# Kernel tuning notes

Measured on AMD Instinct MI355X. Metric: run time of the kernel, lower is better.

## Reference

```python
import jax, jax.numpy as jnp
import numpy as np

B, S, T, E = 16, 512, 128, 256
VIN, VOUT, ENC, DEC = 32000, 32000, 32, 128


def pos_encoding(length, depth):
    # standard sinusoidal positional encoding (TF tutorial / AddPositionalEmbedding)
    half = depth // 2
    pos = jnp.arange(length, dtype=jnp.float32)[:, None]          # (L,1)
    rates = (1.0 / (10000.0 ** (jnp.arange(half, dtype=jnp.float32) / half)))[None, :]
    ang = pos * rates                                             # (L, depth/2)
    return jnp.concatenate([jnp.sin(ang), jnp.cos(ang)], axis=-1)  # (L, depth)


def lstm_scan(x, W, U, b, reverse=False):
    # Keras LSTM, gate order i,f,g,o; zero initial state. x: (B,S,E) -> (B,S,H), h_final
    Bn, H = x.shape[0], U.shape[0]
    def step(carry, xt):
        h, c = carry
        z = xt @ W + h @ U + b
        i, f, g, o = jnp.split(z, 4, axis=-1)
        c = jax.nn.sigmoid(f) * c + jax.nn.sigmoid(i) * jnp.tanh(g)
        h = jax.nn.sigmoid(o) * jnp.tanh(c)
        return (h, c), h
    h0 = jnp.zeros((Bn, H), x.dtype)
    (h, _), hs = jax.lax.scan(step, (h0, h0), jnp.swapaxes(x, 0, 1), reverse=reverse)
    return jnp.swapaxes(hs, 0, 1), h


def setup_inputs() -> dict:
    key = jax.random.key(0)
    ks = jax.random.split(key, 20)
    s = 0.05
    return {
        'source': jax.random.randint(ks[0], (B, S), 0, VIN, dtype=jnp.int32),
        'target': jax.random.randint(ks[1], (B, T), 0, VOUT, dtype=jnp.int32),
        'src_emb': jax.random.normal(ks[2], (VIN, E), jnp.float32) * s,
        'tgt_emb': jax.random.normal(ks[3], (VOUT, E), jnp.float32) * s,
        'Wf': jax.random.normal(ks[4], (E, 4 * ENC), jnp.float32) * s,
        'Uf': jax.random.normal(ks[5], (ENC, 4 * ENC), jnp.float32) * s,
        'bf': jnp.zeros((4 * ENC,), jnp.float32),
        'Wb': jax.random.normal(ks[6], (E, 4 * ENC), jnp.float32) * s,
        'Ub': jax.random.normal(ks[7], (ENC, 4 * ENC), jnp.float32) * s,
        'bb': jnp.zeros((4 * ENC,), jnp.float32),
        'W1': jax.random.normal(ks[8], (2 * ENC, DEC), jnp.float32) * s,
        'b1': jnp.zeros((DEC,), jnp.float32),
        'W2': jax.random.normal(ks[9], (2 * ENC, DEC), jnp.float32) * s,
        'b2': jnp.zeros((DEC,), jnp.float32),
        'Vw': jax.random.normal(ks[10], (DEC, 1), jnp.float32) * s,
        'Vb': jnp.zeros((1,), jnp.float32),
        'Wd': jax.random.normal(ks[11], (2 * ENC + E, 4 * DEC), jnp.float32) * s,
        'bd': jnp.zeros((4 * DEC,), jnp.float32),
        'Wfc': jax.random.normal(ks[12], (DEC, VOUT), jnp.float32) * s,
        'bfc': jnp.zeros((VOUT,), jnp.float32),
    }


def reference(source, target, src_emb, tgt_emb, Wf, Uf, bf, Wb, Ub, bb,
              W1, b1, W2, b2, Vw, Vb, Wd, bd, Wfc, bfc):
    # source embedding + positional encoding
    src = src_emb[source] * jnp.sqrt(jnp.float32(E)) + pos_encoding(S, E)  # (B,S,E)
    # bidirectional encoder (enc_units=32 each direction)
    out_f, hf = lstm_scan(src, Wf, Uf, bf)
    out_b, hb = lstm_scan(src, Wb, Ub, bb, reverse=True)
    enc = jnp.concatenate([out_f, out_b], axis=-1)        # (B,S,64)
    hidden = jnp.concatenate([hf, hb], axis=-1)           # (B,64) — constant query
    # Bahdanau attention with constant query -> constant context vector
    score = jnp.tanh(hidden[:, None, :] @ W1 + b1 + enc @ W2 + b2) @ Vw + Vb  # (B,S,1)
    attw = jax.nn.softmax(score, axis=1)
    ctx = jnp.sum(attw * enc, axis=1)                     # (B,64)
    # per-timestep decoder: LSTM restarts from zero state each step, so all
    # T steps are independent -> vectorize single LSTM step over T
    temb = tgt_emb[target]                                # (B,T,E)
    x = jnp.concatenate(
        [jnp.broadcast_to(ctx[:, None, :], (B, T, 2 * ENC)), temb], axis=-1)  # (B,T,320)
    z = x @ Wd + bd
    i, f, g, o = jnp.split(z, 4, axis=-1)
    c = jax.nn.sigmoid(i) * jnp.tanh(g)                   # c_prev = 0 => forget gate inert
    h = jax.nn.sigmoid(o) * jnp.tanh(c)                   # (B,T,128)
    return h @ Wfc + bfc                                  # (B,T,VOUT)
```

## Files before the change

### kernel.cpp

```cpp
#include <hip/hip_runtime.h>
#include <hip/hip_bf16.h>
#include <math.h>

#define BB 16
#define SS 512
#define TT 128
#define EE 256
#define ENC 32
#define DEC 128
#define VOUT 32000

typedef _Float16 half8 __attribute__((ext_vector_type(8)));
typedef float floatx4 __attribute__((ext_vector_type(4)));

__device__ __forceinline__ float sigmoidf_(float x) { return 1.0f / (1.0f + expf(-x)); }

__global__ __launch_bounds__(256) void k_embed_gemm(
    const int* __restrict__ source, const float* __restrict__ src_emb,
    const float* __restrict__ Wf, const float* __restrict__ bf,
    const float* __restrict__ Wb, const float* __restrict__ bb,
    float* __restrict__ Zf, float* __restrict__ Zb)
{
    __shared__ __align__(16) float sSrc[8][EE];
    const int r0 = blockIdx.x * 8;
    const int tid = threadIdx.x;

    for (int idx = tid; idx < 8 * EE; idx += 256) {
        const int r = idx >> 8, e = idx & 255;
        const int row = r0 + r;
        const int s = row & (SS - 1);
        const int tok = source[row];
        float v = src_emb[(size_t)tok * EE + e] * 16.0f;
        const int jh = (e < 128) ? e : (e - 128);
        const float rate = expf(-0.07195578415f * (float)jh);
        const float ang = (float)s * rate;
        v += (e < 128) ? sinf(ang) : cosf(ang);
        sSrc[r][e] = v;
    }
    __syncthreads();

    const int j = tid & 127;
    const float* W = (tid < 128) ? Wf : Wb;
    const float* bv = (tid < 128) ? bf : bb;
    float* Zo = (tid < 128) ? Zf : Zb;

    float acc[8];
    const float bias = bv[j];
#pragma unroll
    for (int r = 0; r < 8; ++r) acc[r] = bias;

    for (int e = 0; e < EE; e += 4) {
        const float w0 = W[(e + 0) * 128 + j];
        const float w1 = W[(e + 1) * 128 + j];
        const float w2 = W[(e + 2) * 128 + j];
        const float w3 = W[(e + 3) * 128 + j];
#pragma unroll
        for (int r = 0; r < 8; ++r) {
            const float4 x = *(const float4*)&sSrc[r][e];
            acc[r] = fmaf(x.x, w0, acc[r]);
            acc[r] = fmaf(x.y, w1, acc[r]);
            acc[r] = fmaf(x.z, w2, acc[r]);
            acc[r] = fmaf(x.w, w3, acc[r]);
        }
    }
#pragma unroll
    for (int r = 0; r < 8; ++r) Zo[(size_t)(r0 + r) * 128 + j] = acc[r];
}

__global__ __launch_bounds__(128) void k_scan(
    const float* __restrict__ Zf, const float* __restrict__ Zb,
    const float* __restrict__ Uf, const float* __restrict__ Ub,
    float* __restrict__ enc, float* __restrict__ hidden)
{
    const int blk = blockIdx.x;
    const int batch = blk >> 1;
    const int dir = blk & 1;
    const float* Z = dir ? Zb : Zf;
    const float* U = dir ? Ub : Uf;
    const int j = threadIdx.x;

    float u[ENC];
#pragma unroll
    for (int k = 0; k < ENC; ++k) u[k] = U[k * 128 + j];

    __shared__ __align__(16) float sh[ENC];
    __shared__ float sc_[ENC];
    __shared__ float sz[128];
    if (j < ENC) { sh[j] = 0.0f; sc_[j] = 0.0f; }
    __syncthreads();

    const float* Zp = Z + (size_t)batch * (SS * 128) + j;
    float zin = Zp[(dir ? (SS - 1) : 0) * 128];

    for (int step = 0; step < SS; ++step) {
        const int t = dir ? (SS - 1 - step) : step;
        float acc0 = zin;
        if (step < SS - 1) {
            const int tn = dir ? (SS - 2 - step) : (step + 1);
            zin = Zp[tn * 128];
        }
        float acc1 = 0.f, acc2 = 0.f, acc3 = 0.f;
        {
            const float4 h0 = *(const float4*)&sh[0];
            const float4 h1 = *(const float4*)&sh[4];
            const float4 h2 = *(const float4*)&sh[8];
            const float4 h3 = *(const float4*)&sh[12];
            const float4 h4 = *(const float4*)&sh[16];
            const float4 h5 = *(const float4*)&sh[20];
            const float4 h6 = *(const float4*)&sh[24];
            const float4 h7 = *(const float4*)&sh[28];
            acc0 = fmaf(h0.x, u[0], acc0);  acc0 = fmaf(h0.y, u[1], acc0);
            acc0 = fmaf(h0.z, u[2], acc0);  acc0 = fmaf(h0.w, u[3], acc0);
            acc1 = fmaf(h1.x, u[4], acc1);  acc1 = fmaf(h1.y, u[5], acc1);
            acc1 = fmaf(h1.z, u[6], acc1);  acc1 = fmaf(h1.w, u[7], acc1);
            acc2 = fmaf(h2.x, u[8], acc2);  acc2 = fmaf(h2.y, u[9], acc2);
            acc2 = fmaf(h2.z, u[10], acc2); acc2 = fmaf(h2.w, u[11], acc2);
            acc3 = fmaf(h3.x, u[12], acc3); acc3 = fmaf(h3.y, u[13], acc3);
            acc3 = fmaf(h3.z, u[14], acc3); acc3 = fmaf(h3.w, u[15], acc3);
            acc0 = fmaf(h4.x, u[16], acc0); acc0 = fmaf(h4.y, u[17], acc0);
            acc0 = fmaf(h4.z, u[18], acc0); acc0 = fmaf(h4.w, u[19], acc0);
            acc1 = fmaf(h5.x, u[20], acc1); acc1 = fmaf(h5.y, u[21], acc1);
            acc1 = fmaf(h5.z, u[22], acc1); acc1 = fmaf(h5.w, u[23], acc1);
            acc2 = fmaf(h6.x, u[24], acc2); acc2 = fmaf(h6.y, u[25], acc2);
            acc2 = fmaf(h6.z, u[26], acc2); acc2 = fmaf(h6.w, u[27], acc2);
            acc3 = fmaf(h7.x, u[28], acc3); acc3 = fmaf(h7.y, u[29], acc3);
            acc3 = fmaf(h7.z, u[30], acc3); acc3 = fmaf(h7.w, u[31], acc3);
        }
        const float zval = (acc0 + acc1) + (acc2 + acc3);
        const float a = (j < 64 || j >= 96) ? sigmoidf_(zval) : tanhf(zval);
        sz[j] = a;
        __syncthreads();
        if (j < ENC) {
            const float c = sz[32 + j] * sc_[j] + sz[j] * sz[64 + j];
            const float h = sz[96 + j] * tanhf(c);
            sc_[j] = c;
            sh[j] = h;
            enc[((size_t)batch * SS + t) * 64 + dir * ENC + j] = h;
            if (step == SS - 1) hidden[batch * 64 + dir * ENC + j] = h;
        }
        __syncthreads();
    }
}

__global__ __launch_bounds__(128) void k_q(
    const float* __restrict__ hidden, const float* __restrict__ W1,
    const float* __restrict__ b1, const float* __restrict__ b2,
    float* __restrict__ q2)
{
    const int b = blockIdx.x, d = threadIdx.x;
    __shared__ __align__(16) float shid[64];
    if (d < 64) shid[d] = hidden[b * 64 + d];
    __syncthreads();
    float acc = b1[d] + b2[d];
#pragma unroll
    for (int k = 0; k < 64; k += 4) {
        const float4 h4 = *(const float4*)&shid[k];
        acc = fmaf(h4.x, W1[(k + 0) * 128 + d], acc);
        acc = fmaf(h4.y, W1[(k + 1) * 128 + d], acc);
        acc = fmaf(h4.z, W1[(k + 2) * 128 + d], acc);
        acc = fmaf(h4.w, W1[(k + 3) * 128 + d], acc);
    }
    q2[b * 128 + d] = acc;
}

__global__ __launch_bounds__(128) void k_score(
    const float* __restrict__ enc, const float* __restrict__ q2,
    const float* __restrict__ W2, const float* __restrict__ Vw,
    const float* __restrict__ Vb, float* __restrict__ scores)
{
    const int bs = blockIdx.x;
    const int b = bs >> 9;
    const int tid = threadIdx.x;
    __shared__ __align__(16) float se[64];
    __shared__ float sred2[2];
    if (tid < 64) se[tid] = enc[(size_t)bs * 64 + tid];
    __syncthreads();
    float acc = q2[b * 128 + tid];
#pragma unroll
    for (int k = 0; k < 64; k += 4) {
        const float4 e4 = *(const float4*)&se[k];
        acc = fmaf(e4.x, W2[(k + 0) * 128 + tid], acc);
        acc = fmaf(e4.y, W2[(k + 1) * 128 + tid], acc);
        acc = fmaf(e4.z, W2[(k + 2) * 128 + tid], acc);
        acc = fmaf(e4.w, W2[(k + 3) * 128 + tid], acc);
    }
    float v = tanhf(acc) * Vw[tid];
#pragma unroll
    for (int off = 32; off > 0; off >>= 1) v += __shfl_down(v, off);
    if ((tid & 63) == 0) sred2[tid >> 6] = v;
    __syncthreads();
    if (tid == 0) scores[bs] = sred2[0] + sred2[1] + Vb[0];
}

__global__ __launch_bounds__(512) void k_softmax_ctx(
    const float* __restrict__ scores, const float* __restrict__ enc,
    float* __restrict__ ctx)
{
    const int b = blockIdx.x, tid = threadIdx.x;
    __shared__ float sw[SS];
    __shared__ float sred[SS];
    const float sc = scores[b * SS + tid];
    sred[tid] = sc;
    __syncthreads();
    for (int s2 = 256; s2 > 0; s2 >>= 1) {
        if (tid < s2) sred[tid] = fmaxf(sred[tid], sred[tid + s2]);
        __syncthreads();
    }
    const float mx = sred[0];
    __syncthreads();
    const float ex = expf(sc - mx);
    sw[tid] = ex;
    sred[tid] = ex;
    __syncthreads();
    for (int s2 = 256; s2 > 0; s2 >>= 1) {
        if (tid < s2) sred[tid] += sred[tid + s2];
        __syncthreads();
    }
    const float inv = 1.0f / sred[0];
    __syncthreads();
    const int d = tid & 63, chunk = tid >> 6;
    float acc = 0.0f;
    const int sbeg = chunk * 64;
    for (int s = sbeg; s < sbeg + 64; ++s)
        acc = fmaf(sw[s], enc[((size_t)b * SS + s) * 64 + d], acc);
    sred[tid] = acc * inv;
    __syncthreads();
    if (tid < 64) {
        float t = 0.0f;
#pragma unroll
        for (int c = 0; c < 8; ++c) t += sred[c * 64 + tid];
        ctx[b * 64 + tid] = t;
    }
}

__global__ __launch_bounds__(384) void k_dec(
    const int* __restrict__ target, const float* __restrict__ tgt_emb,
    const float* __restrict__ ctx, const float* __restrict__ Wd,
    const float* __restrict__ bd, unsigned short* __restrict__ Ah)
{
    const int bt0 = blockIdx.x * 8;
    const int tid = threadIdx.x;
    __shared__ __align__(16) float sx[8][320];
    __shared__ float sg[3][8][128];

    for (int idx = tid; idx < 8 * 320; idx += 384) {
        const int r = idx / 320, k = idx % 320;
        const int bt = bt0 + r;
        const int b = bt >> 7;
        float v;
        if (k < 64) v = ctx[b * 64 + k];
        else v = tgt_emb[(size_t)target[bt] * EE + (k - 64)];
        sx[r][k] = v;
    }
    __syncthreads();

    const int g = tid >> 7, u = tid & 127;
    const int col = (g == 0) ? u : ((g == 1) ? (256 + u) : (384 + u));
    float acc[8];
    const float bias = bd[col];
#pragma unroll
    for (int r = 0; r < 8; ++r) acc[r] = bias;

#pragma unroll 2
    for (int k = 0; k < 320; k += 4) {
        const float w0 = Wd[(k + 0) * 512 + col];
        const float w1 = Wd[(k + 1) * 512 + col];
        const float w2 = Wd[(k + 2) * 512 + col];
        const float w3 = Wd[(k + 3) * 512 + col];
#pragma unroll
        for (int r = 0; r < 8; ++r) {
            const float4 x = *(const float4*)&sx[r][k];
            acc[r] = fmaf(x.x, w0, acc[r]);
            acc[r] = fmaf(x.y, w1, acc[r]);
            acc[r] = fmaf(x.z, w2, acc[r]);
            acc[r] = fmaf(x.w, w3, acc[r]);
        }
    }
#pragma unroll
    for (int r = 0; r < 8; ++r) {
        const float a = acc[r];
        sg[g][r][u] = (g == 1) ? tanhf(a) : sigmoidf_(a);
    }
    __syncthreads();
    if (tid < 128) {
#pragma unroll
        for (int r = 0; r < 8; ++r) {
            const float i_ = sg[0][r][u];
            const float g_ = sg[1][r][u];
            const float o_ = sg[2][r][u];
            const float h = o_ * tanhf(i_ * g_);
            Ah[(size_t)(bt0 + r) * 128 + u] =
                __builtin_bit_cast(unsigned short, (_Float16)h);
        }
    }
}

__global__ __launch_bounds__(256) void k_cvtB(
    const float* __restrict__ Wfc, unsigned short* __restrict__ Bt)
{
    __shared__ __align__(16) unsigned short sH[64][136];
    const int n0 = blockIdx.x * 64;
    const int tid = threadIdx.x;
    const int kk = tid >> 4;
    const int n4 = tid & 15;

#pragma unroll
    for (int p = 0; p < 8; ++p) {
        const int k = p * 16 + kk;
        const float4 v = *(const float4*)&Wfc[(size_t)k * VOUT + n0 + n4 * 4];
        sH[n4 * 4 + 0][k] = __builtin_bit_cast(unsigned short, (_Float16)v.x);
        sH[n4 * 4 + 1][k] = __builtin_bit_cast(unsigned short, (_Float16)v.y);
        sH[n4 * 4 + 2][k] = __builtin_bit_cast(unsigned short, (_Float16)v.z);
        sH[n4 * 4 + 3][k] = __builtin_bit_cast(unsigned short, (_Float16)v.w);
    }
    __syncthreads();

    const int r0 = tid >> 4;
    const int l8 = (tid & 15) * 8;
#pragma unroll
    for (int p = 0; p < 4; ++p) {
        const int r = p * 16 + r0;
        *(uint4*)&Bt[(size_t)(n0 + r) * 128 + l8] = *(const uint4*)&sH[r][l8];
    }
}

__global__ __launch_bounds__(256) void k_out_f16(
    const unsigned short* __restrict__ Ah,
    const unsigned short* __restrict__ Bt,
    const float* __restrict__ bias, float* __restrict__ C)
{
    const int tid  = threadIdx.x;
    const int wave = tid >> 6;
    const int lane = tid & 63;
    const int wm = wave >> 1, wn = wave & 1;
    const int rb = blockIdx.y * 128 + wm * 64;
    const int cb = blockIdx.x * 128 + wn * 64;
    const int lm = lane & 15;
    const int quad = lane >> 4;

    floatx4 acc[4][4];
#pragma unroll
    for (int nt = 0; nt < 4; ++nt) {
        const float bv = bias[cb + nt * 16 + lm];
#pragma unroll
        for (int mt = 0; mt < 4; ++mt)
            acc[mt][nt] = (floatx4){bv, bv, bv, bv};
    }

    const unsigned short* pA = Ah + (size_t)(rb + lm) * 128 + quad * 8;
    const unsigned short* pB = Bt + (size_t)(cb + lm) * 128 + quad * 8;

#pragma unroll
    for (int kc = 0; kc < 128; kc += 32) {
        half8 af[4], bfr[4];
#pragma unroll
        for (int mt = 0; mt < 4; ++mt)
            af[mt] = *(const half8*)(pA + mt * (16 * 128) + kc);
#pragma unroll
        for (int nt = 0; nt < 4; ++nt)
            bfr[nt] = *(const half8*)(pB + nt * (16 * 128) + kc);
#pragma unroll
        for (int mt = 0; mt < 4; ++mt)
#pragma unroll
            for (int nt = 0; nt < 4; ++nt)
                acc[mt][nt] = __builtin_amdgcn_mfma_f32_16x16x32_f16(
                    af[mt], bfr[nt], acc[mt][nt], 0, 0, 0);
    }

#pragma unroll
    for (int mt = 0; mt < 4; ++mt) {
        const int r0 = rb + mt * 16 + quad * 4;
#pragma unroll
        for (int nt = 0; nt < 4; ++nt) {
            const int col = cb + nt * 16 + lm;
            float* Cp = C + (size_t)r0 * VOUT + col;
#pragma unroll
            for (int r = 0; r < 4; ++r)
                Cp[(size_t)r * VOUT] = acc[mt][nt][r];
        }
    }
}

extern "C" void kernel_launch(void* const* d_in, const int* in_sizes, int n_in,
                              void* d_out, int out_size, void* d_ws, size_t ws_size,
                              hipStream_t stream) {
    (void)in_sizes; (void)n_in; (void)out_size; (void)ws_size;
    const int*   source  = (const int*)  d_in[0];
    const int*   target  = (const int*)  d_in[1];
    const float* src_emb = (const float*)d_in[2];
    const float* tgt_emb = (const float*)d_in[3];
    const float* Wf      = (const float*)d_in[4];
    const float* Uf      = (const float*)d_in[5];
    const float* bf      = (const float*)d_in[6];
    const float* Wb      = (const float*)d_in[7];
    const float* Ub      = (const float*)d_in[8];
    const float* bb      = (const float*)d_in[9];
    const float* W1      = (const float*)d_in[10];
    const float* b1      = (const float*)d_in[11];
    const float* W2      = (const float*)d_in[12];
    const float* b2      = (const float*)d_in[13];
    const float* Vw      = (const float*)d_in[14];
    const float* Vb      = (const float*)d_in[15];
    const float* Wd      = (const float*)d_in[16];
    const float* bd      = (const float*)d_in[17];
    const float* Wfc     = (const float*)d_in[18];
    const float* bfc     = (const float*)d_in[19];
    float* out = (float*)d_out;

    float* ws     = (float*)d_ws;
    float* Zf     = ws;
    float* Zb     = Zf + 1048576;
    float* enc    = Zb + 1048576;
    float* hidden = enc + 524288;
    float* q2     = hidden + 1024;
    float* scores = q2 + 2048;
    float* ctx    = scores + 8192;
    unsigned short* Ah = (unsigned short*)(ctx + 1024);
    unsigned short* Bt = (unsigned short*)Zf;

    k_embed_gemm<<<1024, 256, 0, stream>>>(source, src_emb, Wf, bf, Wb, bb, Zf, Zb);
    k_scan<<<32, 128, 0, stream>>>(Zf, Zb, Uf, Ub, enc, hidden);
    k_q<<<16, 128, 0, stream>>>(hidden, W1, b1, b2, q2);
    k_score<<<8192, 128, 0, stream>>>(enc, q2, W2, Vw, Vb, scores);
    k_softmax_ctx<<<16, 512, 0, stream>>>(scores, enc, ctx);
    k_cvtB<<<500, 256, 0, stream>>>(Wfc, Bt);
    k_dec<<<256, 384, 0, stream>>>(target, tgt_emb, ctx, Wd, bd, Ah);
    k_out_f16<<<dim3(250, 16), 256, 0, stream>>>(Ah, Bt, bfc, out);
}
```

Measured before the change: 751.3 us.

## Run LSTM scan in a single wavefront using readlane instead of shared memory

The recurrent scan kernel moves from 128 threads with shared-memory exchange and two block barriers per step to one 64-lane wavefront. Each lane computes two gate columns, broadcasts h via readlane, and exchanges gates with a cross-half shuffle. Tanh is computed as a scaled sigmoid through fast reciprocal and exp. This removes per-step barriers and LDS round trips from the serial 512-step critical path, at some cost in accuracy from the approximate reciprocal and tanh.

```diff
diff --git a/kernel.cpp b/kernel.cpp
--- a/kernel.cpp
+++ b/kernel.cpp
@@ -14,6 +14,7 @@
 typedef float floatx4 __attribute__((ext_vector_type(4)));
 
 __device__ __forceinline__ float sigmoidf_(float x) { return 1.0f / (1.0f + expf(-x)); }
+__device__ __forceinline__ float rcpf_(float x) { return __builtin_amdgcn_rcpf(x); }
 
 __global__ __launch_bounds__(256) void k_embed_gemm(
     const int* __restrict__ source, const float* __restrict__ src_emb,
@@ -67,7 +68,7 @@
     for (int r = 0; r < 8; ++r) Zo[(size_t)(r0 + r) * 128 + j] = acc[r];
 }
 
-__global__ __launch_bounds__(128) void k_scan(
+__global__ __launch_bounds__(64) void k_scan(
     const float* __restrict__ Zf, const float* __restrict__ Zb,
     const float* __restrict__ Uf, const float* __restrict__ Ub,
     float* __restrict__ enc, float* __restrict__ hidden)
@@ -75,71 +76,80 @@
     const int blk = blockIdx.x;
     const int batch = blk >> 1;
     const int dir = blk & 1;
-    const float* Z = dir ? Zb : Zf;
-    const float* U = dir ? Ub : Uf;
-    const int j = threadIdx.x;
-
-    float u[ENC];
-#pragma unroll
-    for (int k = 0; k < ENC; ++k) u[k] = U[k * 128 + j];
-
-    __shared__ __align__(16) float sh[ENC];
-    __shared__ float sc_[ENC];
-    __shared__ float sz[128];
-    if (j < ENC) { sh[j] = 0.0f; sc_[j] = 0.0f; }
-    __syncthreads();
-
-    const float* Zp = Z + (size_t)batch * (SS * 128) + j;
-    float zin = Zp[(dir ? (SS - 1) : 0) * 128];
+    const float* __restrict__ Z = dir ? Zb : Zf;
+    const float* __restrict__ U = dir ? Ub : Uf;
+    const int lane = threadIdx.x;
+    const int u = lane & 31;
+    const int half = lane >> 5;
+    const int colA = half * 64 + u;
+    const int colB = half * 64 + 32 + u;
+
+    float uA[ENC], uB[ENC];
+#pragma unroll
+    for (int k = 0; k < ENC; ++k) {
+        uA[k] = U[k * 128 + colA];
+        uB[k] = U[k * 128 + colB];
+    }
+
+    const float* __restrict__ Zrow = Z + (size_t)batch * (SS * 128);
+    const int dt = dir ? -1 : 1;
+    int t = dir ? (SS - 1) : 0;
+    float zA = Zrow[t * 128 + colA];
+    float zB = Zrow[t * 128 + colB];
+
+    const float m = half ? 2.0f : 1.0f;
+    const float madd = 1.0f - m;
+
+    float h = 0.0f, c = 0.0f;
 
     for (int step = 0; step < SS; ++step) {
-        const int t = dir ? (SS - 1 - step) : step;
-        float acc0 = zin;
+        float accA0 = zA, accA1 = 0.f, accA2 = 0.f, accA3 = 0.f;
+        float accB0 = zB, accB1 = 0.f, accB2 = 0.f, accB3 = 0.f;
         if (step < SS - 1) {
-            const int tn = dir ? (SS - 2 - step) : (step + 1);
-            zin = Zp[tn * 128];
-        }
-        float acc1 = 0.f, acc2 = 0.f, acc3 = 0.f;
-        {
-            const float4 h0 = *(const float4*)&sh[0];
-            const float4 h1 = *(const float4*)&sh[4];
-            const float4 h2 = *(const float4*)&sh[8];
-            const float4 h3 = *(const float4*)&sh[12];
-            const float4 h4 = *(const float4*)&sh[16];
-            const float4 h5 = *(const float4*)&sh[20];
-            const float4 h6 = *(const float4*)&sh[24];
-            const float4 h7 = *(const float4*)&sh[28];
-            acc0 = fmaf(h0.x, u[0], acc0);  acc0 = fmaf(h0.y, u[1], acc0);
-            acc0 = fmaf(h0.z, u[2], acc0);  acc0 = fmaf(h0.w, u[3], acc0);
-            acc1 = fmaf(h1.x, u[4], acc1);  acc1 = fmaf(h1.y, u[5], acc1);
-            acc1 = fmaf(h1.z, u[6], acc1);  acc1 = fmaf(h1.w, u[7], acc1);
-            acc2 = fmaf(h2.x, u[8], acc2);  acc2 = fmaf(h2.y, u[9], acc2);
-            acc2 = fmaf(h2.z, u[10], acc2); acc2 = fmaf(h2.w, u[11], acc2);
-            acc3 = fmaf(h3.x, u[12], acc3); acc3 = fmaf(h3.y, u[13], acc3);
-            acc3 = fmaf(h3.z, u[14], acc3); acc3 = fmaf(h3.w, u[15], acc3);
-            acc0 = fmaf(h4.x, u[16], acc0); acc0 = fmaf(h4.y, u[17], acc0);
-            acc0 = fmaf(h4.z, u[18], acc0); acc0 = fmaf(h4.w, u[19], acc0);
-            acc1 = fmaf(h5.x, u[20], acc1); acc1 = fmaf(h5.y, u[21], acc1);
-            acc1 = fmaf(h5.z, u[22], acc1); acc1 = fmaf(h5.w, u[23], acc1);
-            acc2 = fmaf(h6.x, u[24], acc2); acc2 = fmaf(h6.y, u[25], acc2);
-            acc2 = fmaf(h6.z, u[26], acc2); acc2 = fmaf(h6.w, u[27], acc2);
-            acc3 = fmaf(h7.x, u[28], acc3); acc3 = fmaf(h7.y, u[29], acc3);
-            acc3 = fmaf(h7.z, u[30], acc3); acc3 = fmaf(h7.w, u[31], acc3);
-        }
-        const float zval = (acc0 + acc1) + (acc2 + acc3);
-        const float a = (j < 64 || j >= 96) ? sigmoidf_(zval) : tanhf(zval);
-        sz[j] = a;
-        __syncthreads();
-        if (j < ENC) {
-            const float c = sz[32 + j] * sc_[j] + sz[j] * sz[64 + j];
-            const float h = sz[96 + j] * tanhf(c);
-            sc_[j] = c;
-            sh[j] = h;
-            enc[((size_t)batch * SS + t) * 64 + dir * ENC + j] = h;
-            if (step == SS - 1) hidden[batch * 64 + dir * ENC + j] = h;
-        }
-        __syncthreads();
-    }
+            const int tn = t + dt;
+            zA = Zrow[tn * 128 + colA];
+            zB = Zrow[tn * 128 + colB];
+        }
+#pragma unroll
+        for (int k = 0; k < ENC; k += 4) {
+            const float h0 = __builtin_bit_cast(float,
+                __builtin_amdgcn_readlane(__builtin_bit_cast(int, h), k + 0));
+            const float h1 = __builtin_bit_cast(float,
+                __builtin_amdgcn_readlane(__builtin_bit_cast(int, h), k + 1));
+            const float h2 = __builtin_bit_cast(float,
+                __builtin_amdgcn_readlane(__builtin_bit_cast(int, h), k + 2));
+            const float h3 = __builtin_bit_cast(float,
+                __builtin_amdgcn_readlane(__builtin_bit_cast(int, h), k + 3));
+            accA0 = fmaf(h0, uA[k + 0], accA0);
+            accB0 = fmaf(h0, uB[k + 0], accB0);
+            accA1 = fmaf(h1, uA[k + 1], accA1);
+            accB1 = fmaf(h1, uB[k + 1], accB1);
+            accA2 = fmaf(h2, uA[k + 2], accA2);
+            accB2 = fmaf(h2, uB[k + 2], accB2);
+            accA3 = fmaf(h3, uA[k + 3], accA3);
+            accB3 = fmaf(h3, uB[k + 3], accB3);
+        }
+        const float zAv = (accA0 + accA1) + (accA2 + accA3);
+        const float zBv = (accB0 + accB1) + (accB2 + accB3);
+
+        const float s1 = rcpf_(1.0f + expf(-m * zAv));
+        const float a1 = fmaf(s1, m, madd);
+        const float a2 = rcpf_(1.0f + expf(-zBv));
+
+        const float t1 = __shfl_xor(a1, 32);
+        const float t2 = __shfl_xor(a2, 32);
+
+        c = fmaf(a2, c, a1 * t1);
+        const float e2 = expf(-2.0f * c);
+        const float tc = (1.0f - e2) * rcpf_(1.0f + e2);
+        h = t2 * tc;
+
+        if (half == 0)
+            enc[((size_t)batch * SS + t) * 64 + dir * ENC + u] = h;
+        t += dt;
+    }
+    if (half == 0)
+        hidden[batch * 64 + dir * ENC + u] = h;
 }
 
 __global__ __launch_bounds__(128) void k_q(
@@ -419,7 +429,7 @@
     unsigned short* Bt = (unsigned short*)Zf;
 
     k_embed_gemm<<<1024, 256, 0, stream>>>(source, src_emb, Wf, bf, Wb, bb, Zf, Zb);
-    k_scan<<<32, 128, 0, stream>>>(Zf, Zb, Uf, Ub, enc, hidden);
+    k_scan<<<32, 64, 0, stream>>>(Zf, Zb, Uf, Ub, enc, hidden);
     k_q<<<16, 128, 0, stream>>>(hidden, W1, b1, b2, q2);
     k_score<<<8192, 128, 0, stream>>>(enc, q2, W2, Vw, Vb, scores);
     k_softmax_ctx<<<16, 512, 0, stream>>>(scores, enc, ctx);
```

After: 639.0 us. 1.18x faster.
